# Kernel tuning notes

Hardware: AMD Instinct MI355X
Metric: run time of the kernel (lower is better)

The kernel has to match this reference:

```python
import jax, jax.numpy as jnp
from jax import lax
import numpy as np

B, T, F = 32, 8192, 16
HID = 128
OUT = 24
K1 = 10


def setup_inputs() -> dict:
    key = jax.random.key(0)
    ks = jax.random.split(key, 5)
    x = jax.random.normal(ks[0], (B, T, F), dtype=jnp.float32)
    # Conv1d(F -> HID, kernel=10): weight (O, I, K), bias (O,)
    w1 = jax.random.normal(ks[1], (HID, F, K1), dtype=jnp.float32) * (1.0 / np.sqrt(F * K1))
    b1 = jax.random.normal(ks[2], (HID,), dtype=jnp.float32) * 0.01
    # Linear(HID*10 -> OUT): weight (OUT, HID*10), bias (OUT,)
    wf = jax.random.normal(ks[3], (OUT, HID * K1), dtype=jnp.float32) * (1.0 / np.sqrt(HID * K1))
    bf = jax.random.normal(ks[4], (OUT,), dtype=jnp.float32) * 0.01
    return {"x": x, "w1": w1, "b1": b1, "wf": wf, "bf": bf}


def reference(x, w1, b1, wf, bf):
    # x: (B, T, F) -> (B, F, T)
    xc = jnp.transpose(x, (0, 2, 1))
    # Conv1d k=10, pad=9 -> length T+9
    h = lax.conv_general_dilated(
        xc, w1, window_strides=(1,), padding=[(9, 9)],
        dimension_numbers=("NCH", "OIH", "NCH")) + b1[None, :, None]  # (B, HID, T+9)
    # out[:, :x.shape[2], :] keeps the first T timesteps
    h = h[:, :, :x.shape[1]]
    h = jnp.concatenate([jnp.repeat(h[:, :, :1], 9, axis=2), h], axis=2)
    # Per-step Linear over flattened 10-step windows == valid conv with k=10.
    # flatten order of window (10, C) is time-major: col index = t*C + c
    kf = jnp.transpose(wf.reshape(wf.shape[0], K1, -1), (0, 2, 1))  # (OUT, HID, 10)
    y = lax.conv_general_dilated(
        h, kf, window_strides=(1,), padding="VALID",
        dimension_numbers=("NCH", "OIH", "NCH")) + bf[None, :, None]  # (B, OUT, T)
    return jnp.transpose(y, (0, 2, 1))  # (B, T, OUT)
```

## Files before the change

### kernel.cpp

```cpp
#include <hip/hip_runtime.h>

#define B_   32
#define T_   8192
#define F_   16
#define OUT_ 24
#define K1_  10
#define ND   19
#define JP   32
#define TB   512
#define WROWS 536
#define H1OFF (WROWS * 8 + 8)

#define WS_BC_OFF   20480
#define WS_E_OFF    20576
#define WS_W1T_OFF  144992

typedef short short8 __attribute__((ext_vector_type(8)));
typedef float float4v __attribute__((ext_vector_type(4)));

__device__ __forceinline__ unsigned short f2bf(float f) {
    unsigned u = __builtin_bit_cast(unsigned, f);
    unsigned r = (u + 0x7fffu + ((u >> 16) & 1u)) >> 16;
    return (unsigned short)r;
}

__device__ __forceinline__ short8 cvt8(float4 f0, float4 f1) {
    short8 v;
    v[0] = (short)f2bf(f0.x); v[1] = (short)f2bf(f0.y);
    v[2] = (short)f2bf(f0.z); v[3] = (short)f2bf(f0.w);
    v[4] = (short)f2bf(f1.x); v[5] = (short)f2bf(f1.y);
    v[6] = (short)f2bf(f1.z); v[7] = (short)f2bf(f1.w);
    return v;
}

__global__ __launch_bounds__(256) void pre_kernel(const float* __restrict__ w1,
                                                  float* __restrict__ w1t,
                                                  unsigned short* __restrict__ w2pk) {
    int bx = blockIdx.x;
    int tid = threadIdx.x;
    if (bx < 80) {
        int idx = bx * 256 + tid;
        float v = w1[idx];
        int c = idx / 160;
        int rem = idx - c * 160;
        int i = rem / 10;
        int k = rem - i * 10;
        w1t[(k * 16 + i) * 128 + c] = v;
    } else {
        int idx = (bx - 80) * 256 + tid;
        ((unsigned*)w2pk)[idx] = 0;
    }
}

__global__ __launch_bounds__(256) void prep_kernel(const float* __restrict__ w1t,
                                                   const float* __restrict__ b1,
                                                   const float* __restrict__ wf,
                                                   const float* __restrict__ bf,
                                                   unsigned short* __restrict__ w2pk,
                                                   float* __restrict__ bcg,
                                                   float* __restrict__ Eg) {
    int tid = threadIdx.x;
    int lane = tid & 63;
    int wid = blockIdx.x * 4 + (tid >> 6);

    if (wid < 456) {
        int j = wid / ND, d = wid % ND;
        float p[16];
#pragma unroll
        for (int i = 0; i < 16; ++i) p[i] = 0.f;
        int klo = d - 9 > 0 ? d - 9 : 0;
        int khi = d < 9 ? d : 9;
        for (int k = klo; k <= khi; ++k) {
            float w0 = wf[j * 1280 + k * 128 + lane];
            float w1v = wf[j * 1280 + k * 128 + 64 + lane];
            const float* wb = w1t + (d - k) * 16 * 128;
#pragma unroll
            for (int i = 0; i < 16; ++i)
                p[i] = fmaf(w0, wb[i * 128 + lane], fmaf(w1v, wb[i * 128 + 64 + lane], p[i]));
        }
#pragma unroll
        for (int i = 0; i < 16; ++i) {
            p[i] += __shfl_xor(p[i], 1);
            p[i] += __shfl_xor(p[i], 2);
            p[i] += __shfl_xor(p[i], 4);
            p[i] += __shfl_xor(p[i], 8);
            p[i] += __shfl_xor(p[i], 16);
            p[i] += __shfl_xor(p[i], 32);
        }
        if (lane < 16) {
            float v = p[0];
#pragma unroll
            for (int i = 1; i < 16; ++i)
                if (lane == i) v = p[i];
            int kk = d * 16 + lane;
            int ks = kk >> 5, r = kk & 31;
            int quad = r >> 3, z = r & 7;
            int tbl = j >> 4, jj = j & 15;
            int lt = jj + quad * 16;
            w2pk[((tbl * 10 + ks) * 64 + lt) * 8 + z] = f2bf(v);
        }
    } else if (wid < 480) {
        int j = wid - 456;
        float s0 = 0.f, s1 = 0.f;
#pragma unroll
        for (int k = 0; k < K1_; ++k) {
            s0 += wf[j * 1280 + k * 128 + lane];
            s1 += wf[j * 1280 + k * 128 + 64 + lane];
        }
        float s = s0 * b1[lane] + s1 * b1[64 + lane];
        s += __shfl_xor(s, 1);
        s += __shfl_xor(s, 2);
        s += __shfl_xor(s, 4);
        s += __shfl_xor(s, 8);
        s += __shfl_xor(s, 16);
        s += __shfl_xor(s, 32);
        if (lane == 0) bcg[j] = bf[j] + s;
    } else {
        int eidx = wid - 480;
        int t = eidx / 216;
        int rem = eidx % 216;
        int j = rem / 9, tau = rem % 9;
        float p[16];
#pragma unroll
        for (int i = 0; i < 16; ++i) p[i] = 0.f;
        for (int k = 0; k < K1_; ++k) {
            int u = t + k - 9; if (u < 0) u = 0;
            if (tau > u) continue;
            int kap = tau + 9 - u;
            float w0 = wf[j * 1280 + k * 128 + lane];
            float w1v = wf[j * 1280 + k * 128 + 64 + lane];
            const float* wb = w1t + kap * 16 * 128;
#pragma unroll
            for (int i = 0; i < 16; ++i)
                p[i] = fmaf(w0, wb[i * 128 + lane], fmaf(w1v, wb[i * 128 + 64 + lane], p[i]));
        }
#pragma unroll
        for (int i = 0; i < 16; ++i) {
            p[i] += __shfl_xor(p[i], 1);
            p[i] += __shfl_xor(p[i], 2);
            p[i] += __shfl_xor(p[i], 4);
            p[i] += __shfl_xor(p[i], 8);
            p[i] += __shfl_xor(p[i], 16);
            p[i] += __shfl_xor(p[i], 32);
        }
        if (lane < 16) {
            float v = p[0];
#pragma unroll
            for (int i = 1; i < 16; ++i)
                if (lane == i) v = p[i];
            Eg[((t * OUT_ + j) * 9 + tau) * 16 + lane] = v;
        }
    }
}

__global__ __launch_bounds__(256, 3) void main_kernel(const float* __restrict__ x,
                                                   const unsigned short* __restrict__ w2pk,
                                                   const float* __restrict__ bcg,
                                                   float* __restrict__ out,
                                                   const float* __restrict__ Eg) {
    int tid = threadIdx.x;
    int b = blockIdx.y;

    if (blockIdx.x == 16) {
        if (tid >= 9 * OUT_) return;
        int t = tid / OUT_, j = tid % OUT_;
        const float4* xv = (const float4*)(x + (long)b * T_ * F_);
        const float4* ev = (const float4*)(Eg + (long)tid * 144);
        float ax = 0.f, ay = 0.f, az = 0.f, aw = 0.f;
#pragma unroll
        for (int q = 0; q < 36; ++q) {
            float4 e = ev[q];
            float4 v = xv[q];
            ax = fmaf(e.x, v.x, ax);
            ay = fmaf(e.y, v.y, ay);
            az = fmaf(e.z, v.z, az);
            aw = fmaf(e.w, v.w, aw);
        }
        out[((long)b * T_ + t) * OUT_ + j] = bcg[j] + ((ax + ay) + (az + aw));
        return;
    }

    __shared__ short xls[2 * WROWS * 8 + 8];
    int t0 = blockIdx.x * TB;

    for (int idx = tid; idx < 2 * WROWS; idx += 256) {
        int h = idx >= WROWS;
        int row = h ? idx - WROWS : idx;
        int t = t0 - 18 + row;
        short8 v = short8{0, 0, 0, 0, 0, 0, 0, 0};
        if (t >= 0 && t < T_) {
            const float4* p = (const float4*)(x + ((long)b * T_ + t) * 16 + h * 8);
            v = cvt8(p[0], p[1]);
        }
        *(short8*)(xls + h * H1OFF + row * 8) = v;
    }

    int lane = tid & 63, w = tid >> 6;
    int t = lane & 15, q = lane >> 4;
    int h = q & 1, qh = q >> 1;

    const unsigned short* pk0 = w2pk + lane * 8;
    const unsigned short* pk1 = w2pk + 5120 + lane * 8;
    short8 W0[10], W1[10];
#pragma unroll
    for (int ks = 0; ks < 10; ++ks) {
        W0[ks] = *(const short8*)(pk0 + ks * 512);
        W1[ks] = *(const short8*)(pk1 + ks * 512);
    }

    __syncthreads();

    const short* ap = xls + h * H1OFF + (w * 128 + t + qh) * 8;

    long outb = (long)b * T_;
    float4 bc0 = *(const float4*)(bcg + q * 4);
    float4 bc1 = (q < 2) ? *(const float4*)(bcg + 16 + q * 4) : make_float4(0.f, 0.f, 0.f, 0.f);
    bool edge = (blockIdx.x == 0);

    float4v acc[4][2];
#pragma unroll 1
    for (int pass = 0; pass < 2; ++pass) {
#pragma unroll
        for (int mt = 0; mt < 4; ++mt) {
            acc[mt][0] = float4v{0.f, 0.f, 0.f, 0.f};
            acc[mt][1] = float4v{0.f, 0.f, 0.f, 0.f};
        }

#pragma unroll
        for (int ks = 0; ks < 10; ++ks) {
#pragma unroll
            for (int mt = 0; mt < 4; ++mt) {
                short8 xf = *(const short8*)(ap + ((pass * 4 + mt) * 16 + 2 * ks) * 8);
                acc[mt][0] = __builtin_amdgcn_mfma_f32_16x16x32_bf16(W0[ks], xf, acc[mt][0], 0, 0, 0);
                acc[mt][1] = __builtin_amdgcn_mfma_f32_16x16x32_bf16(W1[ks], xf, acc[mt][1], 0, 0, 0);
            }
        }

#pragma unroll
        for (int mt = 0; mt < 4; ++mt) {
            int t_out = t0 + w * 128 + (pass * 4 + mt) * 16 + t;
            if (!edge || t_out >= 9) {
                float* o = out + (outb + t_out) * OUT_;
                float4 v0 = make_float4(acc[mt][0][0] + bc0.x, acc[mt][0][1] + bc0.y,
                                        acc[mt][0][2] + bc0.z, acc[mt][0][3] + bc0.w);
                *(float4*)(o + q * 4) = v0;
                if (q < 2) {
                    float4 v1 = make_float4(acc[mt][1][0] + bc1.x, acc[mt][1][1] + bc1.y,
                                            acc[mt][1][2] + bc1.z, acc[mt][1][3] + bc1.w);
                    *(float4*)(o + 16 + q * 4) = v1;
                }
            }
        }
    }
}

extern "C" void kernel_launch(void* const* d_in, const int* in_sizes, int n_in,
                              void* d_out, int out_size, void* d_ws, size_t ws_size,
                              hipStream_t stream) {
    const float* x  = (const float*)d_in[0];
    const float* w1 = (const float*)d_in[1];
    const float* b1 = (const float*)d_in[2];
    const float* wf = (const float*)d_in[3];
    const float* bf = (const float*)d_in[4];
    float* out = (float*)d_out;
    unsigned short* w2pk = (unsigned short*)d_ws;
    float* bcg = (float*)((char*)d_ws + WS_BC_OFF);
    float* Eg  = (float*)((char*)d_ws + WS_E_OFF);
    float* w1t = (float*)((char*)d_ws + WS_W1T_OFF);

    hipLaunchKernelGGL(pre_kernel, dim3(120), dim3(256), 0, stream, w1, w1t, w2pk);
    hipLaunchKernelGGL(prep_kernel, dim3(606), dim3(256), 0, stream,
                       w1t, b1, wf, bf, w2pk, bcg, Eg);
    hipLaunchKernelGGL(main_kernel, dim3(17, B_), dim3(256), 0, stream,
                       x, w2pk, bcg, out, Eg);
}
```

Baseline: 93.67 us.

## Replace edge correction table with rank-one x[0] correction fused into main tiles

The correction for the first nine output steps is rewritten. The padded conv output at those steps differs from the replicated value only through a term proportional to x[0], so the prep kernel now builds a small per-(t,j) vector Q from partial sums of wf and a single w1 tap instead of the full 9-tap E table. The separate edge block in the main kernel (grid column 16) is removed, and the edge tiles add the Q·x[0] correction in their epilogue. This shrinks the prep grid from 606 to 174 blocks and the main grid by one column of blocks. The cost is scalar fp32 dot products in the epilogue of the edge warps.

```diff
diff --git a/kernel.cpp b/kernel.cpp
--- a/kernel.cpp
+++ b/kernel.cpp
@@ -12,7 +12,7 @@
 #define H1OFF (WROWS * 8 + 8)
 
 #define WS_BC_OFF   20480
-#define WS_E_OFF    20576
+#define WS_Q_OFF    20576
 #define WS_W1T_OFF  144992
 
 typedef short short8 __attribute__((ext_vector_type(8)));
@@ -58,7 +58,7 @@
                                                    const float* __restrict__ bf,
                                                    unsigned short* __restrict__ w2pk,
                                                    float* __restrict__ bcg,
-                                                   float* __restrict__ Eg) {
+                                                   float* __restrict__ Qg) {
     int tid = threadIdx.x;
     int lane = tid & 63;
     int wid = blockIdx.x * 4 + (tid >> 6);
@@ -116,24 +116,18 @@
         s += __shfl_xor(s, 32);
         if (lane == 0) bcg[j] = bf[j] + s;
     } else {
-        int eidx = wid - 480;
-        int t = eidx / 216;
-        int rem = eidx % 216;
-        int j = rem / 9, tau = rem % 9;
+        int qidx = wid - 480;
+        int t = qidx / OUT_, j = qidx % OUT_;
+        float s0 = 0.f, s1 = 0.f;
+        for (int k = 0; k <= 8 - t; ++k) {
+            s0 += wf[j * 1280 + k * 128 + lane];
+            s1 += wf[j * 1280 + k * 128 + 64 + lane];
+        }
+        const float* wb = w1t + 144 * 128;
         float p[16];
 #pragma unroll
-        for (int i = 0; i < 16; ++i) p[i] = 0.f;
-        for (int k = 0; k < K1_; ++k) {
-            int u = t + k - 9; if (u < 0) u = 0;
-            if (tau > u) continue;
-            int kap = tau + 9 - u;
-            float w0 = wf[j * 1280 + k * 128 + lane];
-            float w1v = wf[j * 1280 + k * 128 + 64 + lane];
-            const float* wb = w1t + kap * 16 * 128;
-#pragma unroll
-            for (int i = 0; i < 16; ++i)
-                p[i] = fmaf(w0, wb[i * 128 + lane], fmaf(w1v, wb[i * 128 + 64 + lane], p[i]));
-        }
+        for (int i = 0; i < 16; ++i)
+            p[i] = fmaf(s0, wb[i * 128 + lane], s1 * wb[i * 128 + 64 + lane]);
 #pragma unroll
         for (int i = 0; i < 16; ++i) {
             p[i] += __shfl_xor(p[i], 1);
@@ -148,7 +142,7 @@
 #pragma unroll
             for (int i = 1; i < 16; ++i)
                 if (lane == i) v = p[i];
-            Eg[((t * OUT_ + j) * 9 + tau) * 16 + lane] = v;
+            Qg[qidx * 16 + lane] = v;
         }
     }
 }
@@ -157,28 +151,9 @@
                                                    const unsigned short* __restrict__ w2pk,
                                                    const float* __restrict__ bcg,
                                                    float* __restrict__ out,
-                                                   const float* __restrict__ Eg) {
+                                                   const float* __restrict__ Qg) {
     int tid = threadIdx.x;
     int b = blockIdx.y;
-
-    if (blockIdx.x == 16) {
-        if (tid >= 9 * OUT_) return;
-        int t = tid / OUT_, j = tid % OUT_;
-        const float4* xv = (const float4*)(x + (long)b * T_ * F_);
-        const float4* ev = (const float4*)(Eg + (long)tid * 144);
-        float ax = 0.f, ay = 0.f, az = 0.f, aw = 0.f;
-#pragma unroll
-        for (int q = 0; q < 36; ++q) {
-            float4 e = ev[q];
-            float4 v = xv[q];
-            ax = fmaf(e.x, v.x, ax);
-            ay = fmaf(e.y, v.y, ay);
-            az = fmaf(e.z, v.z, az);
-            aw = fmaf(e.w, v.w, aw);
-        }
-        out[((long)b * T_ + t) * OUT_ + j] = bcg[j] + ((ax + ay) + (az + aw));
-        return;
-    }
 
     __shared__ short xls[2 * WROWS * 8 + 8];
     int t0 = blockIdx.x * TB;
@@ -239,17 +214,35 @@
 #pragma unroll
         for (int mt = 0; mt < 4; ++mt) {
             int t_out = t0 + w * 128 + (pass * 4 + mt) * 16 + t;
-            if (!edge || t_out >= 9) {
-                float* o = out + (outb + t_out) * OUT_;
-                float4 v0 = make_float4(acc[mt][0][0] + bc0.x, acc[mt][0][1] + bc0.y,
-                                        acc[mt][0][2] + bc0.z, acc[mt][0][3] + bc0.w);
-                *(float4*)(o + q * 4) = v0;
+            float* o = out + (outb + t_out) * OUT_;
+            float4 v0 = make_float4(acc[mt][0][0] + bc0.x, acc[mt][0][1] + bc0.y,
+                                    acc[mt][0][2] + bc0.z, acc[mt][0][3] + bc0.w);
+            float4 v1 = make_float4(acc[mt][1][0] + bc1.x, acc[mt][1][1] + bc1.y,
+                                    acc[mt][1][2] + bc1.z, acc[mt][1][3] + bc1.w);
+            if (edge && t_out < 9) {
+                const float* x0 = x + (long)b * T_ * F_;
+                const float* Qt = Qg + t_out * OUT_ * 16;
+                float c0[4] = {0.f, 0.f, 0.f, 0.f};
+#pragma unroll
+                for (int r = 0; r < 4; ++r) {
+                    const float* qr = Qt + (q * 4 + r) * 16;
+#pragma unroll
+                    for (int i = 0; i < 16; ++i) c0[r] = fmaf(qr[i], x0[i], c0[r]);
+                }
+                v0.x += c0[0]; v0.y += c0[1]; v0.z += c0[2]; v0.w += c0[3];
                 if (q < 2) {
-                    float4 v1 = make_float4(acc[mt][1][0] + bc1.x, acc[mt][1][1] + bc1.y,
-                                            acc[mt][1][2] + bc1.z, acc[mt][1][3] + bc1.w);
-                    *(float4*)(o + 16 + q * 4) = v1;
+                    float c1[4] = {0.f, 0.f, 0.f, 0.f};
+#pragma unroll
+                    for (int r = 0; r < 4; ++r) {
+                        const float* qr = Qt + (16 + q * 4 + r) * 16;
+#pragma unroll
+                        for (int i = 0; i < 16; ++i) c1[r] = fmaf(qr[i], x0[i], c1[r]);
+                    }
+                    v1.x += c1[0]; v1.y += c1[1]; v1.z += c1[2]; v1.w += c1[3];
                 }
             }
+            *(float4*)(o + q * 4) = v0;
+            if (q < 2) *(float4*)(o + 16 + q * 4) = v1;
         }
     }
 }
@@ -265,12 +258,12 @@
     float* out = (float*)d_out;
     unsigned short* w2pk = (unsigned short*)d_ws;
     float* bcg = (float*)((char*)d_ws + WS_BC_OFF);
-    float* Eg  = (float*)((char*)d_ws + WS_E_OFF);
+    float* Qg  = (float*)((char*)d_ws + WS_Q_OFF);
     float* w1t = (float*)((char*)d_ws + WS_W1T_OFF);
 
     hipLaunchKernelGGL(pre_kernel, dim3(120), dim3(256), 0, stream, w1, w1t, w2pk);
-    hipLaunchKernelGGL(prep_kernel, dim3(606), dim3(256), 0, stream,
-                       w1t, b1, wf, bf, w2pk, bcg, Eg);
-    hipLaunchKernelGGL(main_kernel, dim3(17, B_), dim3(256), 0, stream,
-                       x, w2pk, bcg, out, Eg);
-}
+    hipLaunchKernelGGL(prep_kernel, dim3(174), dim3(256), 0, stream,
+                       w1t, b1, wf, bf, w2pk, bcg, Qg);
+    hipLaunchKernelGGL(main_kernel, dim3(16, B_), dim3(256), 0, stream,
+                       x, w2pk, bcg, out, Qg);
+}
```

After: 91.63 us. -2.2%, faster.
